# Performance work log

Hardware: AMD Instinct MI355X
Metric: run time of the kernel (lower is better)

The kernel has to match this reference:

```python
import jax, jax.numpy as jnp
import numpy as np

DIM = 1024
B, S = 4, 4096

def setup_inputs() -> dict:
    key = jax.random.key(0)
    ks = jax.random.split(key, 8)
    scale = 1.0 / np.sqrt(DIM)
    x = jax.random.normal(ks[0], (B, S, DIM), dtype=jnp.float32)
    Wk = jax.random.normal(ks[1], (DIM, DIM), dtype=jnp.float32) * scale
    Wv = jax.random.normal(ks[2], (DIM, DIM), dtype=jnp.float32) * scale
    Wr = jax.random.normal(ks[3], (DIM, DIM), dtype=jnp.float32) * scale
    Wo = jax.random.normal(ks[4], (DIM, DIM), dtype=jnp.float32) * scale
    time_decay = jax.random.normal(ks[5], (DIM,), dtype=jnp.float32) * 0.01 - 5.0
    time_first = jax.random.normal(ks[6], (DIM,), dtype=jnp.float32) * 0.01
    return {"x": x, "Wk": Wk, "Wv": Wv, "Wr": Wr, "Wo": Wo,
            "time_decay": time_decay, "time_first": time_first}

def reference(x, Wk, Wv, Wr, Wo, time_decay, time_first):
    # Projections (Linear with weight [out, in]: y = x @ W^T)
    k = jnp.einsum('bsd,ed->bse', x, Wk)
    v = jnp.einsum('bsd,ed->bse', x, Wv)
    r = jax.nn.sigmoid(jnp.einsum('bsd,ed->bse', x, Wr))
    w = -jnp.exp(time_decay)          # (D,)
    decay = jnp.exp(w)                # exp(w), per-channel decay in (0,1)
    eu = jnp.exp(time_first)          # exp(u)
    kv = k * v                        # (B, S, D)

    def step(state, kv_t):
        wkv = state + eu * kv_t       # output numerator this step
        new_state = decay * state + kv_t
        return new_state, wkv

    state0 = jnp.zeros((x.shape[0], x.shape[2]), dtype=x.dtype)
    # scan over time axis: move S to leading dim
    _, wkv_seq = jax.lax.scan(step, state0, jnp.swapaxes(kv, 0, 1))  # (S, B, D)
    out = r * jnp.swapaxes(wkv_seq, 0, 1)  # (B, S, D)
    return jnp.einsum('bsd,ed->bse', out, Wo)
```

## Files before the change

### kernel.cpp

```cpp
#include <hip/hip_runtime.h>
#include <hip/hip_bf16.h>

#define DIMD   1024
#define BATCH  4
#define SEQ    4096
#define NTOK   (BATCH * SEQ)
#define CHUNK  64
#define NCHUNK (SEQ / CHUNK)

#define BM 128
#define BN 128
#define BK 32
#define BNF 64

typedef unsigned short ushort_t;
typedef __attribute__((ext_vector_type(8))) __bf16   bf16x8;
typedef __attribute__((ext_vector_type(4))) float    f32x4;
typedef __attribute__((ext_vector_type(8))) ushort_t u16x8;

__device__ __forceinline__ float b2f(ushort_t u) {
    union { unsigned int i; float f; } x;
    x.i = ((unsigned int)u) << 16;
    return x.f;
}

__device__ __forceinline__ ushort_t f2b(float f) {
    union { float f; unsigned int i; } x;
    x.f = f;
    unsigned int r = x.i + 0x7fffu + ((x.i >> 16) & 1u);
    return (ushort_t)(r >> 16);
}

__global__ __launch_bounds__(256)
void conv_f2b(const float* __restrict__ src, ushort_t* __restrict__ dst, int n8)
{
    const int i = blockIdx.x * 256 + threadIdx.x;
    if (i >= n8) return;
    const float4* s4 = (const float4*)src;
    const float4 a = s4[i * 2];
    const float4 b = s4[i * 2 + 1];
    u16x8 o;
    o[0] = f2b(a.x); o[1] = f2b(a.y); o[2] = f2b(a.z); o[3] = f2b(a.w);
    o[4] = f2b(b.x); o[5] = f2b(b.y); o[6] = f2b(b.z); o[7] = f2b(b.w);
    *(u16x8*)(dst + (size_t)i * 8) = o;
}

__global__ __launch_bounds__(256)
void conv_w(const float* __restrict__ W0, const float* __restrict__ W1,
            const float* __restrict__ W2, const float* __restrict__ W3,
            ushort_t* __restrict__ dst)
{
    const int m = blockIdx.y;
    const float* src = (m == 0) ? W0 : (m == 1) ? W1 : (m == 2) ? W2 : W3;
    const int i = blockIdx.x * 256 + threadIdx.x;
    const float4* s4 = (const float4*)src;
    const float4 a = s4[i * 2];
    const float4 b = s4[i * 2 + 1];
    u16x8 o;
    o[0] = f2b(a.x); o[1] = f2b(a.y); o[2] = f2b(a.z); o[3] = f2b(a.w);
    o[4] = f2b(b.x); o[5] = f2b(b.y); o[6] = f2b(b.z); o[7] = f2b(b.w);
    *(u16x8*)(dst + (size_t)m * DIMD * DIMD + (size_t)i * 8) = o;
}

__global__ __launch_bounds__(256, 2)
void gemm_kvr(const ushort_t* __restrict__ A,
              const ushort_t* __restrict__ Wk,
              const ushort_t* __restrict__ Wv,
              const ushort_t* __restrict__ Wr,
              const float* __restrict__ td,
              ushort_t* __restrict__ Okv,
              ushort_t* __restrict__ Or,
              float* __restrict__ cs)
{
    __shared__ __align__(16) ushort_t As[BM * BK];
    __shared__ __align__(16) ushort_t Bk[BNF * BK];
    __shared__ __align__(16) ushort_t Bv[BNF * BK];
    __shared__ __align__(16) ushort_t Br[BNF * BK];

    const int tid  = threadIdx.x;
    const int lane = tid & 63;
    const int wv   = tid >> 6;
    const int wr   = wv >> 1;
    const int wc   = wv & 1;
    const int lrow = lane & 15;
    const int kq   = lane >> 4;

    const int row0 = blockIdx.x * BM;
    const int e0   = blockIdx.y * BNF;

    f32x4 ak[4][2], av[4][2], ar[4][2];
#pragma unroll
    for (int i = 0; i < 4; i++)
#pragma unroll
        for (int j = 0; j < 2; j++) {
            ak[i][j] = f32x4{0.f, 0.f, 0.f, 0.f};
            av[i][j] = f32x4{0.f, 0.f, 0.f, 0.f};
            ar[i][j] = f32x4{0.f, 0.f, 0.f, 0.f};
        }

    for (int kt = 0; kt < DIMD / BK; ++kt) {
        const int k0 = kt * BK;

        __syncthreads();

#pragma unroll
        for (int it = 0; it < 2; ++it) {
            const int chunk = tid + it * 256;
            const int r = chunk >> 2;
            const int c = (chunk & 3) << 3;
            const ushort_t* ga = A + (size_t)(row0 + r) * DIMD + k0 + c;
            __builtin_amdgcn_global_load_lds(
                (__attribute__((address_space(1))) void*)ga,
                (__attribute__((address_space(3))) void*)((char*)As + chunk * 16),
                16, 0, 0);
        }
        {
            const int r = tid >> 2;
            const int c = (tid & 3) << 3;
            const size_t go = (size_t)(e0 + r) * DIMD + k0 + c;
            __builtin_amdgcn_global_load_lds(
                (__attribute__((address_space(1))) void*)(Wk + go),
                (__attribute__((address_space(3))) void*)((char*)Bk + tid * 16),
                16, 0, 0);
            __builtin_amdgcn_global_load_lds(
                (__attribute__((address_space(1))) void*)(Wv + go),
                (__attribute__((address_space(3))) void*)((char*)Bv + tid * 16),
                16, 0, 0);
            __builtin_amdgcn_global_load_lds(
                (__attribute__((address_space(1))) void*)(Wr + go),
                (__attribute__((address_space(3))) void*)((char*)Br + tid * 16),
                16, 0, 0);
        }

        __syncthreads();

        bf16x8 af[4], bk4[2], bv4[2], br4[2];
#pragma unroll
        for (int i = 0; i < 4; i++)
            af[i] = *(const bf16x8*)(As + (wr * 64 + i * 16 + lrow) * BK + kq * 8);
#pragma unroll
        for (int j = 0; j < 2; j++) {
            const int bo = (wc * 32 + j * 16 + lrow) * BK + kq * 8;
            bk4[j] = *(const bf16x8*)(Bk + bo);
            bv4[j] = *(const bf16x8*)(Bv + bo);
            br4[j] = *(const bf16x8*)(Br + bo);
        }

#pragma unroll
        for (int i = 0; i < 4; i++)
#pragma unroll
            for (int j = 0; j < 2; j++) {
                ak[i][j] = __builtin_amdgcn_mfma_f32_16x16x32_bf16(
                    af[i], bk4[j], ak[i][j], 0, 0, 0);
                av[i][j] = __builtin_amdgcn_mfma_f32_16x16x32_bf16(
                    af[i], bv4[j], av[i][j], 0, 0, 0);
                ar[i][j] = __builtin_amdgcn_mfma_f32_16x16x32_bf16(
                    af[i], br4[j], ar[i][j], 0, 0, 0);
            }
    }

#pragma unroll
    for (int i = 0; i < 4; i++)
#pragma unroll
        for (int j = 0; j < 2; j++)
#pragma unroll
            for (int r = 0; r < 4; r++) {
                const int row = row0 + wr * 64 + i * 16 + kq * 4 + r;
                const int col = e0 + wc * 32 + j * 16 + lrow;
                const size_t o = (size_t)row * DIMD + col;
                Okv[o] = f2b(ak[i][j][r] * av[i][j][r]);
                Or[o]  = f2b(1.f / (1.f + __expf(-ar[i][j][r])));
            }

#pragma unroll
    for (int j = 0; j < 2; j++) {
        const int col = e0 + wc * 32 + j * 16 + lrow;
        const float w = -__expf(td[col]);
        float s = 0.f;
#pragma unroll
        for (int i = 0; i < 4; i++)
#pragma unroll
            for (int r = 0; r < 4; r++) {
                const int rl = i * 16 + kq * 4 + r;
                s += __expf(w * (float)(63 - rl)) * ak[i][j][r] * av[i][j][r];
            }
        s += __shfl_xor(s, 16);
        s += __shfl_xor(s, 32);
        if (kq == 0) {
            const int gchunk = (row0 >> 6) + wr;
            cs[(size_t)gchunk * DIMD + col] = s;
        }
    }
}

__global__ __launch_bounds__(256, 2)
void gemm_bt(const ushort_t* __restrict__ A,
             const ushort_t* __restrict__ W,
             float* __restrict__ Of)
{
    __shared__ __align__(16) ushort_t As[BM * BK];
    __shared__ __align__(16) ushort_t Bs[BN * BK];

    const int tid  = threadIdx.x;
    const int lane = tid & 63;
    const int wv   = tid >> 6;
    const int wr   = wv >> 1;
    const int wc   = wv & 1;
    const int lrow = lane & 15;
    const int kq   = lane >> 4;

    const int row0 = blockIdx.x * BM;
    const int e0   = blockIdx.y * BN;

    f32x4 acc[4][4];
#pragma unroll
    for (int i = 0; i < 4; i++)
#pragma unroll
        for (int j = 0; j < 4; j++)
            acc[i][j] = f32x4{0.f, 0.f, 0.f, 0.f};

    for (int kt = 0; kt < DIMD / BK; ++kt) {
        const int k0 = kt * BK;

        __syncthreads();

#pragma unroll
        for (int it = 0; it < 2; ++it) {
            const int chunk = tid + it * 256;
            const int r = chunk >> 2;
            const int c = (chunk & 3) << 3;
            const ushort_t* ga = A + (size_t)(row0 + r) * DIMD + k0 + c;
            const ushort_t* gb = W + (size_t)(e0 + r) * DIMD + k0 + c;
            __builtin_amdgcn_global_load_lds(
                (__attribute__((address_space(1))) void*)ga,
                (__attribute__((address_space(3))) void*)((char*)As + chunk * 16),
                16, 0, 0);
            __builtin_amdgcn_global_load_lds(
                (__attribute__((address_space(1))) void*)gb,
                (__attribute__((address_space(3))) void*)((char*)Bs + chunk * 16),
                16, 0, 0);
        }

        __syncthreads();

        bf16x8 af[4], bfr[4];
#pragma unroll
        for (int i = 0; i < 4; i++)
            af[i] = *(const bf16x8*)(As + (wr * 64 + i * 16 + lrow) * BK + kq * 8);
#pragma unroll
        for (int j = 0; j < 4; j++)
            bfr[j] = *(const bf16x8*)(Bs + (wc * 64 + j * 16 + lrow) * BK + kq * 8);

#pragma unroll
        for (int i = 0; i < 4; i++)
#pragma unroll
            for (int j = 0; j < 4; j++)
                acc[i][j] = __builtin_amdgcn_mfma_f32_16x16x32_bf16(
                    af[i], bfr[j], acc[i][j], 0, 0, 0);
    }

#pragma unroll
    for (int i = 0; i < 4; i++)
#pragma unroll
        for (int j = 0; j < 4; j++)
#pragma unroll
            for (int r = 0; r < 4; r++) {
                const int row = row0 + wr * 64 + i * 16 + kq * 4 + r;
                const int col = e0 + wc * 64 + j * 16 + lrow;
                Of[(size_t)row * DIMD + col] = acc[i][j][r];
            }
}

__global__ __launch_bounds__(256)
void chunk_scan(float* __restrict__ cs, const float* __restrict__ td)
{
    const int idx = blockIdx.x * 256 + threadIdx.x;
    const int d = idx & (DIMD - 1);
    const int b = idx >> 10;

    const float w      = -__expf(td[d]);
    const float decayL = __expf(w * (float)CHUNK);

    float v[NCHUNK];
    const size_t base = ((size_t)b * NCHUNK) * DIMD + d;
#pragma unroll
    for (int c = 0; c < NCHUNK; c++)
        v[c] = cs[base + (size_t)c * DIMD];

    float st = 0.f;
#pragma unroll
    for (int c = 0; c < NCHUNK; c++) {
        const float sc = v[c];
        v[c] = st;
        st = decayL * st + sc;
    }

#pragma unroll
    for (int c = 0; c < NCHUNK; c++)
        cs[base + (size_t)c * DIMD] = v[c];
}

__global__ __launch_bounds__(256)
void emit(const ushort_t* __restrict__ kvb, const ushort_t* __restrict__ rb,
          const float* __restrict__ td, const float* __restrict__ tf,
          const float* __restrict__ cs, ushort_t* __restrict__ op)
{
    const int t  = blockIdx.x * 256 + threadIdx.x;
    const int d0 = (t & (DIMD / 8 - 1)) * 8;
    const int bc = t >> 7;
    const int c  = bc & (NCHUNK - 1);
    const int b  = bc >> 6;

    float decay[8], eu[8], st[8];
#pragma unroll
    for (int j = 0; j < 8; j++) {
        decay[j] = __expf(-__expf(td[d0 + j]));
        eu[j]    = __expf(tf[d0 + j]);
    }
    const float* csp = cs + ((size_t)bc * DIMD + d0);
    const float4 s0 = *(const float4*)csp;
    const float4 s1 = *(const float4*)(csp + 4);
    st[0] = s0.x; st[1] = s0.y; st[2] = s0.z; st[3] = s0.w;
    st[4] = s1.x; st[5] = s1.y; st[6] = s1.z; st[7] = s1.w;

    size_t off = ((size_t)b * SEQ + (size_t)c * CHUNK) * DIMD + d0;
#pragma unroll 8
    for (int i = 0; i < CHUNK; i++) {
        const u16x8 kv8 = *(const u16x8*)(kvb + off);
        const u16x8 r8  = *(const u16x8*)(rb + off);
        u16x8 o8;
#pragma unroll
        for (int j = 0; j < 8; j++) {
            const float kv = b2f(kv8[j]);
            o8[j] = f2b(b2f(r8[j]) * (st[j] + eu[j] * kv));
            st[j] = decay[j] * st[j] + kv;
        }
        *(u16x8*)(op + off) = o8;
        off += DIMD;
    }
}

extern "C" void kernel_launch(void* const* d_in, const int* in_sizes, int n_in,
                              void* d_out, int out_size, void* d_ws, size_t ws_size,
                              hipStream_t stream)
{
    const float* x  = (const float*)d_in[0];
    const float* Wk = (const float*)d_in[1];
    const float* Wv = (const float*)d_in[2];
    const float* Wr = (const float*)d_in[3];
    const float* Wo = (const float*)d_in[4];
    const float* td = (const float*)d_in[5];
    const float* tf = (const float*)d_in[6];

    ushort_t* xb  = (ushort_t*)d_ws;
    ushort_t* Wb  = xb + (size_t)NTOK * DIMD;
    ushort_t* Wkb = Wb;
    ushort_t* Wvb = Wb + (size_t)DIMD * DIMD;
    ushort_t* Wrb = Wb + 2 * (size_t)DIMD * DIMD;
    ushort_t* Wob = Wb + 3 * (size_t)DIMD * DIMD;
    float*    cs  = (float*)(Wb + 4 * (size_t)DIMD * DIMD);
    ushort_t* pbuf = xb;

    ushort_t* kvb = (ushort_t*)d_out;
    ushort_t* rb  = kvb + (size_t)NTOK * DIMD;
    float*    out = (float*)d_out;

    conv_f2b<<<NTOK * DIMD / 8 / 256, 256, 0, stream>>>(x, xb, NTOK * DIMD / 8);
    conv_w<<<dim3(DIMD * DIMD / 8 / 256, 4), 256, 0, stream>>>(Wk, Wv, Wr, Wo, Wb);

    gemm_kvr<<<dim3(NTOK / BM, DIMD / BNF), 256, 0, stream>>>(
        xb, Wkb, Wvb, Wrb, td, kvb, rb, cs);

    chunk_scan<<<BATCH * DIMD / 256, 256, 0, stream>>>(cs, td);

    emit<<<BATCH * NCHUNK * (DIMD / 8) / 256, 256, 0, stream>>>(
        kvb, rb, td, tf, cs, pbuf);

    gemm_bt<<<dim3(NTOK / BM, DIMD / BN), 256, 0, stream>>>(pbuf, Wob, out);
}
```

Measured before the change: 314.5 us.

## Retile GEMMs with triple-buffered swizzled LDS, merge converts, fold chunk scan into emit

Both GEMMs move to 256x256-scale tiles with 512-thread blocks, a three-stage global_load_lds pipeline controlled by explicit vmcnt waits, and an XOR-swizzled LDS layout meant to avoid bank conflicts. The K/V/R projection is split into heterogeneous blocks in one launch: some compute k and v (kv product plus chunk sums), others compute r with sigmoid. The input and weight conversion kernels are merged into a single launch, and the separate chunk-scan kernel is removed: each emit thread now recomputes its chunk's prefix state by looping over earlier chunk sums. This cuts launches and raises MFMA reuse per loaded byte. In exchange it uses more registers and LDS per block, and emit does redundant serial work that grows with the chunk index.

```diff
diff --git a/kernel.cpp b/kernel.cpp
--- a/kernel.cpp
+++ b/kernel.cpp
@@ -8,10 +8,8 @@
 #define CHUNK  64
 #define NCHUNK (SEQ / CHUNK)
 
-#define BM 128
-#define BN 128
-#define BK 32
-#define BNF 64
+#define KB2    32
+#define NK2    (DIMD / KB2)
 
 typedef unsigned short ushort_t;
 typedef __attribute__((ext_vector_type(8))) __bf16   bf16x8;
@@ -31,11 +29,31 @@
     return (ushort_t)(r >> 16);
 }
 
+#define GLL(gsrc, ldst) __builtin_amdgcn_global_load_lds( \
+    (__attribute__((address_space(1))) void*)(gsrc), \
+    (__attribute__((address_space(3))) void*)(ldst), 16, 0, 0)
+
 __global__ __launch_bounds__(256)
-void conv_f2b(const float* __restrict__ src, ushort_t* __restrict__ dst, int n8)
+void conv_all(const float* __restrict__ x,
+              const float* __restrict__ W0, const float* __restrict__ W1,
+              const float* __restrict__ W2, const float* __restrict__ W3,
+              ushort_t* __restrict__ xb, ushort_t* __restrict__ wb)
 {
-    const int i = blockIdx.x * 256 + threadIdx.x;
-    if (i >= n8) return;
+    const int id = blockIdx.x;
+    const float* src;
+    ushort_t* dst;
+    int i;
+    if (id < 8192) {
+        i   = id * 256 + threadIdx.x;
+        src = x;
+        dst = xb;
+    } else {
+        const int wid = id - 8192;
+        const int m   = wid >> 9;
+        i   = (wid & 511) * 256 + threadIdx.x;
+        src = (m == 0) ? W0 : (m == 1) ? W1 : (m == 2) ? W2 : W3;
+        dst = wb + (size_t)m * DIMD * DIMD;
+    }
     const float4* s4 = (const float4*)src;
     const float4 a = s4[i * 2];
     const float4 b = s4[i * 2 + 1];
@@ -45,283 +63,324 @@
     *(u16x8*)(dst + (size_t)i * 8) = o;
 }
 
-__global__ __launch_bounds__(256)
-void conv_w(const float* __restrict__ W0, const float* __restrict__ W1,
-            const float* __restrict__ W2, const float* __restrict__ W3,
-            ushort_t* __restrict__ dst)
+__global__ __launch_bounds__(512, 2)
+void gemm_kvrs(const ushort_t* __restrict__ A,
+               const ushort_t* __restrict__ Wk,
+               const ushort_t* __restrict__ Wv,
+               const ushort_t* __restrict__ Wr,
+               const float* __restrict__ td,
+               ushort_t* __restrict__ Okv,
+               ushort_t* __restrict__ Or,
+               float* __restrict__ cs)
 {
-    const int m = blockIdx.y;
-    const float* src = (m == 0) ? W0 : (m == 1) ? W1 : (m == 2) ? W2 : W3;
-    const int i = blockIdx.x * 256 + threadIdx.x;
-    const float4* s4 = (const float4*)src;
-    const float4 a = s4[i * 2];
-    const float4 b = s4[i * 2 + 1];
-    u16x8 o;
-    o[0] = f2b(a.x); o[1] = f2b(a.y); o[2] = f2b(a.z); o[3] = f2b(a.w);
-    o[4] = f2b(b.x); o[5] = f2b(b.y); o[6] = f2b(b.z); o[7] = f2b(b.w);
-    *(u16x8*)(dst + (size_t)m * DIMD * DIMD + (size_t)i * 8) = o;
-}
-
-__global__ __launch_bounds__(256, 2)
-void gemm_kvr(const ushort_t* __restrict__ A,
-              const ushort_t* __restrict__ Wk,
-              const ushort_t* __restrict__ Wv,
-              const ushort_t* __restrict__ Wr,
-              const float* __restrict__ td,
-              ushort_t* __restrict__ Okv,
-              ushort_t* __restrict__ Or,
-              float* __restrict__ cs)
-{
-    __shared__ __align__(16) ushort_t As[BM * BK];
-    __shared__ __align__(16) ushort_t Bk[BNF * BK];
-    __shared__ __align__(16) ushort_t Bv[BNF * BK];
-    __shared__ __align__(16) ushort_t Br[BNF * BK];
+    __shared__ __align__(16) ushort_t smem[49152];
 
     const int tid  = threadIdx.x;
     const int lane = tid & 63;
     const int wv   = tid >> 6;
-    const int wr   = wv >> 1;
-    const int wc   = wv & 1;
     const int lrow = lane & 15;
     const int kq   = lane >> 4;
-
-    const int row0 = blockIdx.x * BM;
-    const int e0   = blockIdx.y * BNF;
-
-    f32x4 ak[4][2], av[4][2], ar[4][2];
-#pragma unroll
-    for (int i = 0; i < 4; i++)
-#pragma unroll
-        for (int j = 0; j < 2; j++) {
-            ak[i][j] = f32x4{0.f, 0.f, 0.f, 0.f};
-            av[i][j] = f32x4{0.f, 0.f, 0.f, 0.f};
-            ar[i][j] = f32x4{0.f, 0.f, 0.f, 0.f};
+    const int swr  = ((kq ^ ((lrow >> 1) & 3))) * 8;
+
+    const int rS = tid >> 2;
+    const int gS = ((tid & 3) ^ ((rS >> 1) & 3)) * 8;
+
+    if (blockIdx.x < 512) {
+        ushort_t* As_[3] = { smem,         smem + 8192,  smem + 16384 };
+        ushort_t* Bk_[3] = { smem + 24576, smem + 28672, smem + 32768 };
+        ushort_t* Bv_[3] = { smem + 36864, smem + 40960, smem + 45056 };
+
+        const int wr   = wv >> 1;
+        const int wc   = wv & 1;
+        const int row0 = (blockIdx.x & 63) * 256;
+        const int e0   = (blockIdx.x >> 6) * 128;
+
+        const size_t aoffs = (size_t)(row0 + rS) * DIMD + gS;
+        const size_t boffs = (size_t)(e0 + rS) * DIMD + gS;
+
+#define KV_STAGE(Aab, Akb, Avb, k0) do { \
+    GLL(A  + aoffs + (k0),                        (char*)(Aab) + tid * 16); \
+    GLL(A  + aoffs + (size_t)128 * DIMD + (k0),   (char*)(Aab) + (tid + 512) * 16); \
+    GLL(Wk + boffs + (k0),                        (char*)(Akb) + tid * 16); \
+    GLL(Wv + boffs + (k0),                        (char*)(Avb) + tid * 16); \
+} while (0)
+
+        f32x4 ak[4][4], av[4][4];
+#pragma unroll
+        for (int i = 0; i < 4; i++)
+#pragma unroll
+            for (int j = 0; j < 4; j++) {
+                ak[i][j] = f32x4{0.f, 0.f, 0.f, 0.f};
+                av[i][j] = f32x4{0.f, 0.f, 0.f, 0.f};
+            }
+
+        KV_STAGE(As_[0], Bk_[0], Bv_[0], 0);
+        KV_STAGE(As_[1], Bk_[1], Bv_[1], KB2);
+        asm volatile("s_waitcnt vmcnt(4)" ::: "memory");
+        __builtin_amdgcn_s_barrier();
+        asm volatile("" ::: "memory");
+
+        ushort_t *Aa = As_[0], *Ab = As_[1], *Ac = As_[2];
+        ushort_t *Ka = Bk_[0], *Kb = Bk_[1], *Kc = Bk_[2];
+        ushort_t *Va = Bv_[0], *Vb = Bv_[1], *Vc = Bv_[2];
+
+        for (int t = 0; t < NK2; ++t) {
+            if (t + 2 < NK2) KV_STAGE(Ac, Kc, Vc, (t + 2) * KB2);
+
+            bf16x8 af[4], kb4[4], vb4[4];
+#pragma unroll
+            for (int i = 0; i < 4; i++)
+                af[i] = *(const bf16x8*)(Aa + (wr * 64 + i * 16 + lrow) * KB2 + swr);
+#pragma unroll
+            for (int j = 0; j < 4; j++) {
+                const int bo = (wc * 64 + j * 16 + lrow) * KB2 + swr;
+                kb4[j] = *(const bf16x8*)(Ka + bo);
+                vb4[j] = *(const bf16x8*)(Va + bo);
+            }
+#pragma unroll
+            for (int i = 0; i < 4; i++)
+#pragma unroll
+                for (int j = 0; j < 4; j++) {
+                    ak[i][j] = __builtin_amdgcn_mfma_f32_16x16x32_bf16(af[i], kb4[j], ak[i][j], 0, 0, 0);
+                    av[i][j] = __builtin_amdgcn_mfma_f32_16x16x32_bf16(af[i], vb4[j], av[i][j], 0, 0, 0);
+                }
+
+            if (t + 2 < NK2) asm volatile("s_waitcnt vmcnt(4)" ::: "memory");
+            else             asm volatile("s_waitcnt vmcnt(0)" ::: "memory");
+            __builtin_amdgcn_s_barrier();
+            asm volatile("" ::: "memory");
+            ushort_t* tp;
+            tp = Aa; Aa = Ab; Ab = Ac; Ac = tp;
+            tp = Ka; Ka = Kb; Kb = Kc; Kc = tp;
+            tp = Va; Va = Vb; Vb = Vc; Vc = tp;
         }
 
-    for (int kt = 0; kt < DIMD / BK; ++kt) {
-        const int k0 = kt * BK;
-
-        __syncthreads();
-
-#pragma unroll
-        for (int it = 0; it < 2; ++it) {
-            const int chunk = tid + it * 256;
-            const int r = chunk >> 2;
-            const int c = (chunk & 3) << 3;
-            const ushort_t* ga = A + (size_t)(row0 + r) * DIMD + k0 + c;
-            __builtin_amdgcn_global_load_lds(
-                (__attribute__((address_space(1))) void*)ga,
-                (__attribute__((address_space(3))) void*)((char*)As + chunk * 16),
-                16, 0, 0);
+#pragma unroll
+        for (int i = 0; i < 4; i++)
+#pragma unroll
+            for (int j = 0; j < 4; j++)
+#pragma unroll
+                for (int r = 0; r < 4; r++) {
+                    const int row = row0 + wr * 64 + i * 16 + kq * 4 + r;
+                    const int col = e0 + wc * 64 + j * 16 + lrow;
+                    Okv[(size_t)row * DIMD + col] = f2b(ak[i][j][r] * av[i][j][r]);
+                }
+
+#pragma unroll
+        for (int j = 0; j < 4; j++) {
+            const int col = e0 + wc * 64 + j * 16 + lrow;
+            const float w = -__expf(td[col]);
+            float s = 0.f;
+#pragma unroll
+            for (int i = 0; i < 4; i++)
+#pragma unroll
+                for (int r = 0; r < 4; r++) {
+                    const int rl = i * 16 + kq * 4 + r;
+                    s += __expf(w * (float)(63 - rl)) * ak[i][j][r] * av[i][j][r];
+                }
+            s += __shfl_xor(s, 16);
+            s += __shfl_xor(s, 32);
+            if (kq == 0) {
+                const int gchunk = (row0 >> 6) + wr;
+                cs[(size_t)gchunk * DIMD + col] = s;
+            }
         }
-        {
-            const int r = tid >> 2;
-            const int c = (tid & 3) << 3;
-            const size_t go = (size_t)(e0 + r) * DIMD + k0 + c;
-            __builtin_amdgcn_global_load_lds(
-                (__attribute__((address_space(1))) void*)(Wk + go),
-                (__attribute__((address_space(3))) void*)((char*)Bk + tid * 16),
-                16, 0, 0);
-            __builtin_amdgcn_global_load_lds(
-                (__attribute__((address_space(1))) void*)(Wv + go),
-                (__attribute__((address_space(3))) void*)((char*)Bv + tid * 16),
-                16, 0, 0);
-            __builtin_amdgcn_global_load_lds(
-                (__attribute__((address_space(1))) void*)(Wr + go),
-                (__attribute__((address_space(3))) void*)((char*)Br + tid * 16),
-                16, 0, 0);
+#undef KV_STAGE
+    } else {
+        ushort_t* As_[3] = { smem,         smem + 8192,  smem + 16384 };
+        ushort_t* Bs_[3] = { smem + 24576, smem + 32768, smem + 40960 };
+
+        const int id2  = blockIdx.x - 512;
+        const int wr   = wv >> 2;
+        const int wc   = wv & 3;
+        const int row0 = (id2 & 63) * 256;
+        const int e0   = (id2 >> 6) * 256;
+
+        const size_t aoffs = (size_t)(row0 + rS) * DIMD + gS;
+        const size_t boffs = (size_t)(e0 + rS) * DIMD + gS;
+
+#define RS_STAGE(Aab, Bsb, k0) do { \
+    GLL(A  + aoffs + (k0),                      (char*)(Aab) + tid * 16); \
+    GLL(A  + aoffs + (size_t)128 * DIMD + (k0), (char*)(Aab) + (tid + 512) * 16); \
+    GLL(Wr + boffs + (k0),                      (char*)(Bsb) + tid * 16); \
+    GLL(Wr + boffs + (size_t)128 * DIMD + (k0), (char*)(Bsb) + (tid + 512) * 16); \
+} while (0)
+
+        f32x4 acc[8][4];
+#pragma unroll
+        for (int i = 0; i < 8; i++)
+#pragma unroll
+            for (int j = 0; j < 4; j++)
+                acc[i][j] = f32x4{0.f, 0.f, 0.f, 0.f};
+
+        RS_STAGE(As_[0], Bs_[0], 0);
+        RS_STAGE(As_[1], Bs_[1], KB2);
+        asm volatile("s_waitcnt vmcnt(4)" ::: "memory");
+        __builtin_amdgcn_s_barrier();
+        asm volatile("" ::: "memory");
+
+        ushort_t *Aa = As_[0], *Ab = As_[1], *Ac = As_[2];
+        ushort_t *Ba = Bs_[0], *Bb = Bs_[1], *Bc = Bs_[2];
+
+        for (int t = 0; t < NK2; ++t) {
+            if (t + 2 < NK2) RS_STAGE(Ac, Bc, (t + 2) * KB2);
+
+            bf16x8 af[8], bf4[4];
+#pragma unroll
+            for (int i = 0; i < 8; i++)
+                af[i] = *(const bf16x8*)(Aa + (wr * 128 + i * 16 + lrow) * KB2 + swr);
+#pragma unroll
+            for (int j = 0; j < 4; j++)
+                bf4[j] = *(const bf16x8*)(Ba + (wc * 64 + j * 16 + lrow) * KB2 + swr);
+#pragma unroll
+            for (int i = 0; i < 8; i++)
+#pragma unroll
+                for (int j = 0; j < 4; j++)
+                    acc[i][j] = __builtin_amdgcn_mfma_f32_16x16x32_bf16(af[i], bf4[j], acc[i][j], 0, 0, 0);
+
+            if (t + 2 < NK2) asm volatile("s_waitcnt vmcnt(4)" ::: "memory");
+            else             asm volatile("s_waitcnt vmcnt(0)" ::: "memory");
+            __builtin_amdgcn_s_barrier();
+            asm volatile("" ::: "memory");
+            ushort_t* tp;
+            tp = Aa; Aa = Ab; Ab = Ac; Ac = tp;
+            tp = Ba; Ba = Bb; Bb = Bc; Bc = tp;
         }
 
-        __syncthreads();
-
-        bf16x8 af[4], bk4[2], bv4[2], br4[2];
-#pragma unroll
-        for (int i = 0; i < 4; i++)
-            af[i] = *(const bf16x8*)(As + (wr * 64 + i * 16 + lrow) * BK + kq * 8);
-#pragma unroll
-        for (int j = 0; j < 2; j++) {
-            const int bo = (wc * 32 + j * 16 + lrow) * BK + kq * 8;
-            bk4[j] = *(const bf16x8*)(Bk + bo);
-            bv4[j] = *(const bf16x8*)(Bv + bo);
-            br4[j] = *(const bf16x8*)(Br + bo);
-        }
-
-#pragma unroll
-        for (int i = 0; i < 4; i++)
-#pragma unroll
-            for (int j = 0; j < 2; j++) {
-                ak[i][j] = __builtin_amdgcn_mfma_f32_16x16x32_bf16(
-                    af[i], bk4[j], ak[i][j], 0, 0, 0);
-                av[i][j] = __builtin_amdgcn_mfma_f32_16x16x32_bf16(
-                    af[i], bv4[j], av[i][j], 0, 0, 0);
-                ar[i][j] = __builtin_amdgcn_mfma_f32_16x16x32_bf16(
-                    af[i], br4[j], ar[i][j], 0, 0, 0);
-            }
-    }
-
-#pragma unroll
-    for (int i = 0; i < 4; i++)
-#pragma unroll
-        for (int j = 0; j < 2; j++)
-#pragma unroll
-            for (int r = 0; r < 4; r++) {
-                const int row = row0 + wr * 64 + i * 16 + kq * 4 + r;
-                const int col = e0 + wc * 32 + j * 16 + lrow;
-                const size_t o = (size_t)row * DIMD + col;
-                Okv[o] = f2b(ak[i][j][r] * av[i][j][r]);
-                Or[o]  = f2b(1.f / (1.f + __expf(-ar[i][j][r])));
-            }
-
-#pragma unroll
-    for (int j = 0; j < 2; j++) {
-        const int col = e0 + wc * 32 + j * 16 + lrow;
-        const float w = -__expf(td[col]);
-        float s = 0.f;
-#pragma unroll
-        for (int i = 0; i < 4; i++)
-#pragma unroll
-            for (int r = 0; r < 4; r++) {
-                const int rl = i * 16 + kq * 4 + r;
-                s += __expf(w * (float)(63 - rl)) * ak[i][j][r] * av[i][j][r];
-            }
-        s += __shfl_xor(s, 16);
-        s += __shfl_xor(s, 32);
-        if (kq == 0) {
-            const int gchunk = (row0 >> 6) + wr;
-            cs[(size_t)gchunk * DIMD + col] = s;
-        }
-    }
-}
-
-__global__ __launch_bounds__(256, 2)
+#pragma unroll
+        for (int i = 0; i < 8; i++)
+#pragma unroll
+            for (int j = 0; j < 4; j++)
+#pragma unroll
+                for (int r = 0; r < 4; r++) {
+                    const int row = row0 + wr * 128 + i * 16 + kq * 4 + r;
+                    const int col = e0 + wc * 64 + j * 16 + lrow;
+                    Or[(size_t)row * DIMD + col] =
+                        f2b(1.f / (1.f + __expf(-acc[i][j][r])));
+                }
+#undef RS_STAGE
+    }
+}
+
+__global__ __launch_bounds__(512, 2)
 void gemm_bt(const ushort_t* __restrict__ A,
              const ushort_t* __restrict__ W,
              float* __restrict__ Of)
 {
-    __shared__ __align__(16) ushort_t As[BM * BK];
-    __shared__ __align__(16) ushort_t Bs[BN * BK];
+    __shared__ __align__(16) ushort_t smem[49152];
 
     const int tid  = threadIdx.x;
     const int lane = tid & 63;
     const int wv   = tid >> 6;
-    const int wr   = wv >> 1;
-    const int wc   = wv & 1;
+    const int wr   = wv >> 2;
+    const int wc   = wv & 3;
     const int lrow = lane & 15;
     const int kq   = lane >> 4;
-
-    const int row0 = blockIdx.x * BM;
-    const int e0   = blockIdx.y * BN;
-
-    f32x4 acc[4][4];
-#pragma unroll
-    for (int i = 0; i < 4; i++)
+    const int swr  = ((kq ^ ((lrow >> 1) & 3))) * 8;
+
+    const int rS = tid >> 2;
+    const int gS = ((tid & 3) ^ ((rS >> 1) & 3)) * 8;
+
+    const int row0 = blockIdx.x * 256;
+    const int e0   = blockIdx.y * 256;
+
+    const size_t aoffs = (size_t)(row0 + rS) * DIMD + gS;
+    const size_t boffs = (size_t)(e0 + rS) * DIMD + gS;
+
+    ushort_t* As_[3] = { smem,         smem + 8192,  smem + 16384 };
+    ushort_t* Bs_[3] = { smem + 24576, smem + 32768, smem + 40960 };
+
+#define BT_STAGE(Aab, Bsb, k0) do { \
+    GLL(A + aoffs + (k0),                      (char*)(Aab) + tid * 16); \
+    GLL(A + aoffs + (size_t)128 * DIMD + (k0), (char*)(Aab) + (tid + 512) * 16); \
+    GLL(W + boffs + (k0),                      (char*)(Bsb) + tid * 16); \
+    GLL(W + boffs + (size_t)128 * DIMD + (k0), (char*)(Bsb) + (tid + 512) * 16); \
+} while (0)
+
+    f32x4 acc[8][4];
+#pragma unroll
+    for (int i = 0; i < 8; i++)
 #pragma unroll
         for (int j = 0; j < 4; j++)
             acc[i][j] = f32x4{0.f, 0.f, 0.f, 0.f};
 
-    for (int kt = 0; kt < DIMD / BK; ++kt) {
-        const int k0 = kt * BK;
-
-        __syncthreads();
-
-#pragma unroll
-        for (int it = 0; it < 2; ++it) {
-            const int chunk = tid + it * 256;
-            const int r = chunk >> 2;
-            const int c = (chunk & 3) << 3;
-            const ushort_t* ga = A + (size_t)(row0 + r) * DIMD + k0 + c;
-            const ushort_t* gb = W + (size_t)(e0 + r) * DIMD + k0 + c;
-            __builtin_amdgcn_global_load_lds(
-                (__attribute__((address_space(1))) void*)ga,
-                (__attribute__((address_space(3))) void*)((char*)As + chunk * 16),
-                16, 0, 0);
-            __builtin_amdgcn_global_load_lds(
-                (__attribute__((address_space(1))) void*)gb,
-                (__attribute__((address_space(3))) void*)((char*)Bs + chunk * 16),
-                16, 0, 0);
-        }
-
-        __syncthreads();
-
-        bf16x8 af[4], bfr[4];
-#pragma unroll
-        for (int i = 0; i < 4; i++)
-            af[i] = *(const bf16x8*)(As + (wr * 64 + i * 16 + lrow) * BK + kq * 8);
+    BT_STAGE(As_[0], Bs_[0], 0);
+    BT_STAGE(As_[1], Bs_[1], KB2);
+    asm volatile("s_waitcnt vmcnt(4)" ::: "memory");
+    __builtin_amdgcn_s_barrier();
+    asm volatile("" ::: "memory");
+
+    ushort_t *Aa = As_[0], *Ab = As_[1], *Ac = As_[2];
+    ushort_t *Ba = Bs_[0], *Bb = Bs_[1], *Bc = Bs_[2];
+
+    for (int t = 0; t < NK2; ++t) {
+        if (t + 2 < NK2) BT_STAGE(Ac, Bc, (t + 2) * KB2);
+
+        bf16x8 af[8], bf4[4];
+#pragma unroll
+        for (int i = 0; i < 8; i++)
+            af[i] = *(const bf16x8*)(Aa + (wr * 128 + i * 16 + lrow) * KB2 + swr);
 #pragma unroll
         for (int j = 0; j < 4; j++)
-            bfr[j] = *(const bf16x8*)(Bs + (wc * 64 + j * 16 + lrow) * BK + kq * 8);
-
-#pragma unroll
-        for (int i = 0; i < 4; i++)
+            bf4[j] = *(const bf16x8*)(Ba + (wc * 64 + j * 16 + lrow) * KB2 + swr);
+#pragma unroll
+        for (int i = 0; i < 8; i++)
 #pragma unroll
             for (int j = 0; j < 4; j++)
-                acc[i][j] = __builtin_amdgcn_mfma_f32_16x16x32_bf16(
-                    af[i], bfr[j], acc[i][j], 0, 0, 0);
-    }
-
-#pragma unroll
-    for (int i = 0; i < 4; i++)
+                acc[i][j] = __builtin_amdgcn_mfma_f32_16x16x32_bf16(af[i], bf4[j], acc[i][j], 0, 0, 0);
+
+        if (t + 2 < NK2) asm volatile("s_waitcnt vmcnt(4)" ::: "memory");
+        else             asm volatile("s_waitcnt vmcnt(0)" ::: "memory");
+        __builtin_amdgcn_s_barrier();
+        asm volatile("" ::: "memory");
+        ushort_t* tp;
+        tp = Aa; Aa = Ab; Ab = Ac; Ac = tp;
+        tp = Ba; Ba = Bb; Bb = Bc; Bc = tp;
+    }
+
+#pragma unroll
+    for (int i = 0; i < 8; i++)
 #pragma unroll
         for (int j = 0; j < 4; j++)
 #pragma unroll
             for (int r = 0; r < 4; r++) {
-                const int row = row0 + wr * 64 + i * 16 + kq * 4 + r;
+                const int row = row0 + wr * 128 + i * 16 + kq * 4 + r;
                 const int col = e0 + wc * 64 + j * 16 + lrow;
                 Of[(size_t)row * DIMD + col] = acc[i][j][r];
             }
-}
-
-__global__ __launch_bounds__(256)
-void chunk_scan(float* __restrict__ cs, const float* __restrict__ td)
-{
-    const int idx = blockIdx.x * 256 + threadIdx.x;
-    const int d = idx & (DIMD - 1);
-    const int b = idx >> 10;
-
-    const float w      = -__expf(td[d]);
-    const float decayL = __expf(w * (float)CHUNK);
-
-    float v[NCHUNK];
-    const size_t base = ((size_t)b * NCHUNK) * DIMD + d;
-#pragma unroll
-    for (int c = 0; c < NCHUNK; c++)
-        v[c] = cs[base + (size_t)c * DIMD];
-
-    float st = 0.f;
-#pragma unroll
-    for (int c = 0; c < NCHUNK; c++) {
-        const float sc = v[c];
-        v[c] = st;
-        st = decayL * st + sc;
-    }
-
-#pragma unroll
-    for (int c = 0; c < NCHUNK; c++)
-        cs[base + (size_t)c * DIMD] = v[c];
-}
-
-__global__ __launch_bounds__(256)
+#undef BT_STAGE
+}
+
+__global__ __launch_bounds__(64)
 void emit(const ushort_t* __restrict__ kvb, const ushort_t* __restrict__ rb,
           const float* __restrict__ td, const float* __restrict__ tf,
           const float* __restrict__ cs, ushort_t* __restrict__ op)
 {
-    const int t  = blockIdx.x * 256 + threadIdx.x;
+    const int t  = blockIdx.x * 64 + threadIdx.x;
     const int d0 = (t & (DIMD / 8 - 1)) * 8;
     const int bc = t >> 7;
     const int c  = bc & (NCHUNK - 1);
     const int b  = bc >> 6;
 
-    float decay[8], eu[8], st[8];
+    float decay[8], eu[8], dL[8], st[8];
 #pragma unroll
     for (int j = 0; j < 8; j++) {
-        decay[j] = __expf(-__expf(td[d0 + j]));
+        const float w = -__expf(td[d0 + j]);
+        decay[j] = __expf(w);
+        dL[j]    = __expf(w * (float)CHUNK);
         eu[j]    = __expf(tf[d0 + j]);
-    }
-    const float* csp = cs + ((size_t)bc * DIMD + d0);
-    const float4 s0 = *(const float4*)csp;
-    const float4 s1 = *(const float4*)(csp + 4);
-    st[0] = s0.x; st[1] = s0.y; st[2] = s0.z; st[3] = s0.w;
-    st[4] = s1.x; st[5] = s1.y; st[6] = s1.z; st[7] = s1.w;
+        st[j]    = 0.f;
+    }
+
+    const float* csb = cs + ((size_t)b * NCHUNK) * DIMD + d0;
+    for (int cp = 0; cp < c; cp++) {
+        const float4 s0 = *(const float4*)(csb + (size_t)cp * DIMD);
+        const float4 s1 = *(const float4*)(csb + (size_t)cp * DIMD + 4);
+        st[0] = dL[0] * st[0] + s0.x; st[1] = dL[1] * st[1] + s0.y;
+        st[2] = dL[2] * st[2] + s0.z; st[3] = dL[3] * st[3] + s0.w;
+        st[4] = dL[4] * st[4] + s1.x; st[5] = dL[5] * st[5] + s1.y;
+        st[6] = dL[6] * st[6] + s1.z; st[7] = dL[7] * st[7] + s1.w;
+    }
 
     size_t off = ((size_t)b * SEQ + (size_t)c * CHUNK) * DIMD + d0;
 #pragma unroll 8
@@ -365,16 +424,13 @@
     ushort_t* rb  = kvb + (size_t)NTOK * DIMD;
     float*    out = (float*)d_out;
 
-    conv_f2b<<<NTOK * DIMD / 8 / 256, 256, 0, stream>>>(x, xb, NTOK * DIMD / 8);
-    conv_w<<<dim3(DIMD * DIMD / 8 / 256, 4), 256, 0, stream>>>(Wk, Wv, Wr, Wo, Wb);
-
-    gemm_kvr<<<dim3(NTOK / BM, DIMD / BNF), 256, 0, stream>>>(
+    conv_all<<<8192 + 2048, 256, 0, stream>>>(x, Wk, Wv, Wr, Wo, xb, Wb);
+
+    gemm_kvrs<<<512 + 256, 512, 0, stream>>>(
         xb, Wkb, Wvb, Wrb, td, kvb, rb, cs);
 
-    chunk_scan<<<BATCH * DIMD / 256, 256, 0, stream>>>(cs, td);
-
-    emit<<<BATCH * NCHUNK * (DIMD / 8) / 256, 256, 0, stream>>>(
+    emit<<<BATCH * NCHUNK * (DIMD / 8) / 64, 64, 0, stream>>>(
         kvb, rb, td, tf, cs, pbuf);
 
-    gemm_bt<<<dim3(NTOK / BM, DIMD / BN), 256, 0, stream>>>(pbuf, Wob, out);
-}
+    gemm_bt<<<dim3(NTOK / 256, DIMD / 256), 512, 0, stream>>>(pbuf, Wob, out);
+}
```

Result: no change. 311.2 us (-1.0%).
